# Kernel tuning notes

Measured on AMD Instinct MI355X. Metric: run time of the kernel, lower is better.

## Reference

```python
import jax, jax.numpy as jnp
import numpy as np

DIM = 384
HEADS = 12
CUBE = (4, 7, 7)
N = CUBE[0] * CUBE[1] * CUBE[2]  # 196
HIDDEN = 4 * DIM
BW = 256  # num_windows * batch
EPS = 1e-5


def _relative_position_index():
    c, h, w = CUBE
    coords = np.stack(np.meshgrid(np.arange(c), np.arange(h), np.arange(w), indexing='ij'))  # [3,c,h,w]
    flat = coords.reshape(3, -1)  # [3, N]
    rel = flat[:, :, None] - flat[:, None, :]  # [3, N, N]
    rel = rel.transpose(1, 2, 0).copy()
    rel[:, :, 0] += c - 1
    rel[:, :, 1] += h - 1
    rel[:, :, 2] += w - 1
    rel[:, :, 1] *= 2 * w - 1
    rel[:, :, 0] *= (2 * h - 1) * (2 * w - 1)
    return rel.sum(-1).astype(np.int32)  # [N, N]


def setup_inputs() -> dict:
    key = jax.random.key(0)
    ks = jax.random.split(key, 16)
    s = 0.02
    table_rows = (2 * CUBE[0] - 1) * (2 * CUBE[1] - 1) * (2 * CUBE[2] - 1)
    return {
        'x': jax.random.normal(ks[0], (BW, N, DIM), jnp.float32),
        'norm1_w': jnp.ones((DIM,), jnp.float32),
        'norm1_b': jnp.zeros((DIM,), jnp.float32),
        'qkv_w': jax.random.normal(ks[1], (DIM, 3 * DIM), jnp.float32) * s,
        'qkv_b': jnp.zeros((3 * DIM,), jnp.float32),
        'proj_w': jax.random.normal(ks[2], (DIM, DIM), jnp.float32) * s,
        'proj_b': jnp.zeros((DIM,), jnp.float32),
        'rpb_table': jax.random.normal(ks[3], (table_rows, HEADS), jnp.float32) * s,
        'norm2_w': jnp.ones((DIM,), jnp.float32),
        'norm2_b': jnp.zeros((DIM,), jnp.float32),
        'fc1_w': jax.random.normal(ks[4], (DIM, HIDDEN), jnp.float32) * s,
        'fc1_b': jnp.zeros((HIDDEN,), jnp.float32),
        'fc2_w': jax.random.normal(ks[5], (HIDDEN, DIM), jnp.float32) * s,
        'fc2_b': jnp.zeros((DIM,), jnp.float32),
        'rpi': jnp.asarray(_relative_position_index()),
    }


def _layernorm(x, w, b):
    mu = jnp.mean(x, axis=-1, keepdims=True)
    var = jnp.mean(jnp.square(x - mu), axis=-1, keepdims=True)
    return (x - mu) * jax.lax.rsqrt(var + EPS) * w + b


def reference(x, norm1_w, norm1_b, qkv_w, qkv_b, proj_w, proj_b, rpb_table,
              norm2_w, norm2_b, fc1_w, fc1_b, fc2_w, fc2_b, rpi):
    B_, n, C = x.shape
    hd = C // HEADS
    scale = hd ** (-0.5)

    # --- attention branch ---
    h = _layernorm(x, norm1_w, norm1_b)
    qkv = (h @ qkv_w + qkv_b).reshape(B_, n, 3, HEADS, hd)
    q, k, v = qkv[:, :, 0], qkv[:, :, 1], qkv[:, :, 2]  # [B_, n, H, hd]
    attn = jnp.einsum('bqhd,bkhd->bhqk', q * scale, k)
    bias = rpb_table[rpi]                 # [n, n, H]
    attn = attn + jnp.transpose(bias, (2, 0, 1))[None]
    attn = jax.nn.softmax(attn, axis=-1)
    out = jnp.einsum('bhqk,bkhd->bqhd', attn, v).reshape(B_, n, C)
    out = out @ proj_w + proj_b
    x = x + out

    # --- MLP branch ---
    h = _layernorm(x, norm2_w, norm2_b)
    h = jax.nn.gelu(h @ fc1_w + fc1_b, approximate=False)
    h = h @ fc2_w + fc2_b
    return x + h
```

## Files before the change

kernel.cpp:

```cpp
#include <hip/hip_runtime.h>
#include <hip/hip_bf16.h>
#include <math.h>

#define NDIM 384
#define NHEADS 12
#define NTOK 196
#define NBATCH 256
#define M_TOK (NBATCH * NTOK)
#define NHID 1536
#define THREE_DIM 1152
#define HD 32
#define EPSV 1e-5f
#define BH_STRIDE 7168
#define BPAD 224
#define LOG2E 1.4426950408889634f

typedef __hip_bfloat16 bf16;
typedef __attribute__((ext_vector_type(8))) short short8;
typedef __attribute__((ext_vector_type(4))) short short4v;
typedef __attribute__((ext_vector_type(4))) float f32x4;

__device__ __forceinline__ void gload_lds16(const void* g, void* l) {
  __builtin_amdgcn_global_load_lds((const __attribute__((address_space(1))) void*)g,
                                   (__attribute__((address_space(3))) void*)l, 16, 0, 0);
}

__global__ void k_transpose_bf16(const float* __restrict__ src, bf16* __restrict__ dst,
                                 int K, int N) {
  int idx = blockIdx.x * 256 + threadIdx.x;
  if (idx >= K * N) return;
  int k = idx / N, n = idx - k * N;
  dst[n * K + k] = __float2bfloat16(src[idx]);
}

__global__ void k_build_bias(const float* __restrict__ table, const int* __restrict__ rpi,
                             float* __restrict__ bias_pad) {
  int idx = blockIdx.x * 256 + threadIdx.x;
  if (idx >= NHEADS * BPAD * BPAD) return;
  int h = idx / (BPAD * BPAD);
  int rem = idx - h * (BPAD * BPAD);
  int r = rem / BPAD, c = rem - r * BPAD;
  float v;
  if (c >= NTOK) {
    v = -1e30f;
  } else {
    int rr = r < NTOK ? r : NTOK - 1;
    v = table[rpi[rr * NTOK + c] * NHEADS + h] * LOG2E;
  }
  bias_pad[idx] = v;
}

__global__ __launch_bounds__(256) void k_layernorm(const float* __restrict__ x,
                                                   const float* __restrict__ w,
                                                   const float* __restrict__ b,
                                                   bf16* __restrict__ out) {
  int token = blockIdx.x * 4 + (threadIdx.x >> 6);
  int lane = threadIdx.x & 63;
  const float* xr = x + (size_t)token * NDIM;
  float v[6];
  float s = 0.f;
#pragma unroll
  for (int i = 0; i < 6; ++i) { v[i] = xr[lane + i * 64]; s += v[i]; }
#pragma unroll
  for (int off = 32; off >= 1; off >>= 1) s += __shfl_xor(s, off);
  float mu = s * (1.f / NDIM);
  float s2 = 0.f;
#pragma unroll
  for (int i = 0; i < 6; ++i) { float d = v[i] - mu; s2 += d * d; }
#pragma unroll
  for (int off = 32; off >= 1; off >>= 1) s2 += __shfl_xor(s2, off);
  float r = rsqrtf(s2 * (1.f / NDIM) + EPSV);
  bf16* orow = out + (size_t)token * NDIM;
#pragma unroll
  for (int i = 0; i < 6; ++i) {
    int c = lane + i * 64;
    orow[c] = __float2bfloat16((v[i] - mu) * r * w[c] + b[c]);
  }
}

template <int EPI>
__device__ __forceinline__ void gemm_epilogue(const f32x4 acc[4][4], int m0, int n0,
                                              int lo, int hi,
                                              const float* __restrict__ bias,
                                              const float* __restrict__ resid,
                                              void* __restrict__ Cout,
                                              bf16* __restrict__ pq,
                                              bf16* __restrict__ pk,
                                              bf16* __restrict__ pv, int Nn) {
  const float qscale = 0.17677669529663687f * LOG2E;
#pragma unroll
  for (int i = 0; i < 4; ++i) {
    int r = m0 + i * 16 + lo;
#pragma unroll
    for (int j = 0; j < 4; ++j) {
      int cb0 = n0 + j * 16 + hi * 4;
      f32x4 bv = *(const f32x4*)(bias + cb0);
      f32x4 v;
#pragma unroll
      for (int e = 0; e < 4; ++e) v[e] = acc[i][j][e] + bv[e];
      if (EPI == 3) {
        int d0 = cb0 & 31;
        int hseg = cb0 >> 5;
        int which = hseg / 12;
        int h = hseg - which * 12;
        int b = r / 196;
        int t = r - b * 196;
        size_t base = (size_t)(b * 12 + h) * BH_STRIDE;
        if (which == 2) {
#pragma unroll
          for (int e = 0; e < 4; ++e)
            pv[base + (d0 + e) * BPAD + t] = __float2bfloat16(v[e]);
        } else if (which == 1) {
          union { short4v s; bf16 x[4]; } pack;
#pragma unroll
          for (int e = 0; e < 4; ++e) pack.x[e] = __float2bfloat16(v[e]);
          *(short4v*)(pk + base + t * 32 + d0) = pack.s;
        } else {
          union { short4v s; bf16 x[4]; } pack;
#pragma unroll
          for (int e = 0; e < 4; ++e) pack.x[e] = __float2bfloat16(v[e] * qscale);
          *(short4v*)(pq + base + t * 32 + d0) = pack.s;
        }
      } else if (EPI == 2) {
        size_t idx = (size_t)r * Nn + cb0;
        f32x4 rs = *(const f32x4*)(resid + idx);
#pragma unroll
        for (int e = 0; e < 4; ++e) v[e] += rs[e];
        *(f32x4*)((float*)Cout + idx) = v;
      } else {
        if (EPI == 1) {
#pragma unroll
          for (int e = 0; e < 4; ++e) {
            float val = v[e];
            float t = val * val;
            float p = __builtin_fmaf(0.044715f * val, t, val);
            float E = __expf(1.5957691216057308f * p);
            float rr = __builtin_amdgcn_rcpf(E + 1.f);
            v[e] = val - val * rr;
          }
        }
        union { short4v s; bf16 x[4]; } pack;
#pragma unroll
        for (int e = 0; e < 4; ++e) pack.x[e] = __float2bfloat16(v[e]);
        size_t idx = (size_t)r * Nn + cb0;
        *(short4v*)((bf16*)Cout + idx) = pack.s;
      }
    }
  }
}

template <int EPI>
__global__ __launch_bounds__(512) void k_gemm_bt(const bf16* __restrict__ A,
                                                 const bf16* __restrict__ Bt,
                                                 const float* __restrict__ bias,
                                                 const float* __restrict__ resid,
                                                 void* __restrict__ Cout,
                                                 bf16* __restrict__ pq,
                                                 bf16* __restrict__ pk,
                                                 bf16* __restrict__ pv,
                                                 int Nn, int K, int nbx) {
  __shared__ __align__(16) bf16 As[2][8192];
  __shared__ __align__(16) bf16 Bs[2][4096];
  const int tid = threadIdx.x;
  const int wave = tid >> 6, lane = tid & 63;
  const int lo = lane & 15, hi = lane >> 4;
  const int wm = wave >> 1, wn = wave & 1;

  const int nwg = gridDim.x;
  const int xcd = blockIdx.x & 7, bidx = blockIdx.x >> 3;
  const int q = nwg >> 3, rr8 = nwg & 7;
  const int swz = (xcd < rr8 ? xcd * (q + 1) : rr8 * (q + 1) + (xcd - rr8) * q) + bidx;
  const int m0 = (swz / nbx) * 256, n0 = (swz % nbx) * 128;

  f32x4 acc[4][4];
#pragma unroll
  for (int i = 0; i < 4; ++i)
#pragma unroll
    for (int j = 0; j < 4; ++j) acc[i][j] = (f32x4){0.f, 0.f, 0.f, 0.f};

  const int rowA0 = tid >> 2, part = tid & 3;
  const int sw = part ^ ((rowA0 >> 1) & 3);
  const bf16* ArowP0 = A + (size_t)(m0 + rowA0) * K + sw * 8;
  const bf16* ArowP1 = A + (size_t)(m0 + 128 + rowA0) * K + sw * 8;
  const bf16* BrowP = Bt + (size_t)(n0 + rowA0) * K + sw * 8;

#define STAGE(ks, abuf, bbuf)                                   \
  {                                                             \
    int k0_ = (ks) << 5;                                        \
    gload_lds16(ArowP0 + k0_, (abuf) + tid * 8);                \
    gload_lds16(ArowP1 + k0_, (abuf) + (512 + tid) * 8);        \
    gload_lds16(BrowP + k0_, (bbuf) + tid * 8);                 \
  }

  const int nk = K >> 5;
  STAGE(0, As[0], Bs[0]);
  __syncthreads();

  const int rsw = (lo >> 1) & 3;
  int cur = 0;
  for (int ks = 0; ks < nk; ++ks) {
    if (ks + 1 < nk) STAGE(ks + 1, As[cur ^ 1], Bs[cur ^ 1]);
    short8 af[4], bfr[4];
#pragma unroll
    for (int i = 0; i < 4; ++i) {
      af[i] = *(const short8*)(As[cur] + (wm * 64 + i * 16 + lo) * 32 + (hi ^ rsw) * 8);
      bfr[i] = *(const short8*)(Bs[cur] + (wn * 64 + i * 16 + lo) * 32 + (hi ^ rsw) * 8);
    }
#pragma unroll
    for (int i = 0; i < 4; ++i)
#pragma unroll
      for (int j = 0; j < 4; ++j)
        acc[i][j] = __builtin_amdgcn_mfma_f32_16x16x32_bf16(bfr[j], af[i], acc[i][j], 0, 0, 0);
    __syncthreads();
    cur ^= 1;
  }
#undef STAGE

  gemm_epilogue<EPI>(acc, m0 + wm * 64, n0 + wn * 64, lo, hi, bias, resid, Cout,
                     pq, pk, pv, Nn);
}

__global__ __launch_bounds__(256) void k_attn(const bf16* __restrict__ Qp,
                                              const bf16* __restrict__ Kp,
                                              const bf16* __restrict__ Vtp,
                                              const float* __restrict__ bias_pad,
                                              bf16* __restrict__ out) {
  __shared__ __align__(16) bf16 Ps[4][16][232];
  const int tid = threadIdx.x;
  const int wave = tid >> 6, lane = tid & 63;
  const int lo = lane & 15, hi = lane >> 4;
  const int nwg = gridDim.x;
  const int swz = (blockIdx.x & 7) * (nwg >> 3) + (blockIdx.x >> 3);
  const int unit = swz * 4 + wave;
  const int bh = unit / 13;
  const int qt = unit - bh * 13;
  const int h = bh % 12;
  const int b = bh / 12;
  const bf16* Qb = Qp + (size_t)bh * BH_STRIDE;
  const bf16* Kb = Kp + (size_t)bh * BH_STRIDE;
  const bf16* Vb = Vtp + (size_t)bh * BH_STRIDE;

  for (int i = lane; i < 256; i += 64)
    Ps[wave][i >> 4][208 + (i & 15)] = __float2bfloat16(0.f);

  short8 qf = *(const short8*)(Qb + (qt * 16 + lo) * 32 + hi * 8);

  f32x4 s[13];
  __builtin_amdgcn_s_setprio(1);
#pragma unroll
  for (int kt = 0; kt < 13; ++kt) {
    short8 kf = *(const short8*)(Kb + (kt * 16 + lo) * 32 + hi * 8);
    f32x4 z = {0.f, 0.f, 0.f, 0.f};
    s[kt] = __builtin_amdgcn_mfma_f32_16x16x32_bf16(qf, kf, z, 0, 0, 0);
  }
  __builtin_amdgcn_s_setprio(0);

  f32x4 inv;
#pragma unroll
  for (int e = 0; e < 4; ++e) {
    int qg = qt * 16 + hi * 4 + e;
    const float* brow = bias_pad + ((size_t)h * BPAD + qg) * BPAD;
    float sm = 0.f;
#pragma unroll
    for (int kt = 0; kt < 13; ++kt) {
      float pe = __builtin_amdgcn_exp2f(s[kt][e] + brow[kt * 16 + lo]);
      s[kt][e] = pe;
      sm += pe;
    }
#pragma unroll
    for (int off = 8; off >= 1; off >>= 1) sm += __shfl_xor(sm, off);
    inv[e] = 1.f / sm;
  }

#pragma unroll
  for (int kt = 0; kt < 13; ++kt) {
#pragma unroll
    for (int e = 0; e < 4; ++e)
      Ps[wave][hi * 4 + e][kt * 16 + lo] = __float2bfloat16(s[kt][e]);
  }

  f32x4 o[2] = {{0.f, 0.f, 0.f, 0.f}, {0.f, 0.f, 0.f, 0.f}};
  __builtin_amdgcn_s_setprio(1);
#pragma unroll
  for (int c = 0; c < 7; ++c) {
    short8 pa = *(const short8*)(&Ps[wave][lo][c * 32 + hi * 8]);
#pragma unroll
    for (int n = 0; n < 2; ++n) {
      short8 vf = *(const short8*)(Vb + (n * 16 + lo) * BPAD + c * 32 + hi * 8);
      o[n] = __builtin_amdgcn_mfma_f32_16x16x32_bf16(pa, vf, o[n], 0, 0, 0);
    }
  }
  __builtin_amdgcn_s_setprio(0);

#pragma unroll
  for (int n = 0; n < 2; ++n) {
#pragma unroll
    for (int e = 0; e < 4; ++e) {
      int qg = qt * 16 + hi * 4 + e;
      if (qg < NTOK)
        out[(size_t)(b * NTOK + qg) * NDIM + h * HD + n * 16 + lo] =
            __float2bfloat16(o[n][e] * inv[e]);
    }
  }
}

extern "C" void kernel_launch(void* const* d_in, const int* in_sizes, int n_in,
                              void* d_out, int out_size, void* d_ws, size_t ws_size,
                              hipStream_t stream) {
  const float* x       = (const float*)d_in[0];
  const float* norm1_w = (const float*)d_in[1];
  const float* norm1_b = (const float*)d_in[2];
  const float* qkv_w   = (const float*)d_in[3];
  const float* qkv_b   = (const float*)d_in[4];
  const float* proj_w  = (const float*)d_in[5];
  const float* proj_b  = (const float*)d_in[6];
  const float* rpb     = (const float*)d_in[7];
  const float* norm2_w = (const float*)d_in[8];
  const float* norm2_b = (const float*)d_in[9];
  const float* fc1_w   = (const float*)d_in[10];
  const float* fc1_b   = (const float*)d_in[11];
  const float* fc2_w   = (const float*)d_in[12];
  const float* fc2_b   = (const float*)d_in[13];
  const int*   rpi     = (const int*)d_in[14];
  float* out = (float*)d_out;

  char* ws = (char*)d_ws;
  bf16* pad_q = (bf16*)ws;
  bf16* pad_k = (bf16*)(ws + 44040192);
  bf16* pad_v = (bf16*)(ws + 2 * 44040192);
  float* bias_pad = (float*)(ws + 3 * 44040192);
  bf16* mlp1 = (bf16*)ws;
  bf16* hbuf = (bf16*)(ws + 154140672);
  bf16* wqkv_t = (bf16*)(ws + 154140672 + 38535168);
  bf16* wproj_t = wqkv_t + 442368;
  bf16* wfc1_t = wproj_t + 147456;
  bf16* wfc2_t = wfc1_t + 589824;

  k_transpose_bf16<<<(442368 + 255) / 256, 256, 0, stream>>>(qkv_w, wqkv_t, 384, 1152);
  k_transpose_bf16<<<(147456 + 255) / 256, 256, 0, stream>>>(proj_w, wproj_t, 384, 384);
  k_transpose_bf16<<<(589824 + 255) / 256, 256, 0, stream>>>(fc1_w, wfc1_t, 384, 1536);
  k_transpose_bf16<<<(589824 + 255) / 256, 256, 0, stream>>>(fc2_w, wfc2_t, 1536, 384);
  k_build_bias<<<(NHEADS * BPAD * BPAD + 255) / 256, 256, 0, stream>>>(rpb, rpi, bias_pad);

  k_layernorm<<<M_TOK / 4, 256, 0, stream>>>(x, norm1_w, norm1_b, hbuf);
  k_gemm_bt<3><<<196 * 9, 512, 0, stream>>>(hbuf, wqkv_t, qkv_b, nullptr, nullptr,
                                            pad_q, pad_k, pad_v, 1152, 384, 9);
  k_attn<<<9984, 256, 0, stream>>>(pad_q, pad_k, pad_v, bias_pad, hbuf);
  k_gemm_bt<2><<<196 * 3, 512, 0, stream>>>(hbuf, wproj_t, proj_b, x, out,
                                            nullptr, nullptr, nullptr, 384, 384, 3);
  k_layernorm<<<M_TOK / 4, 256, 0, stream>>>(out, norm2_w, norm2_b, hbuf);
  k_gemm_bt<1><<<196 * 12, 512, 0, stream>>>(hbuf, wfc1_t, fc1_b, nullptr, mlp1,
                                             nullptr, nullptr, nullptr, 1536, 384, 12);
  k_gemm_bt<2><<<196 * 3, 512, 0, stream>>>(mlp1, wfc2_t, fc2_b, out, out,
                                            nullptr, nullptr, nullptr, 384, 1536, 3);
}
```

Measured before the change: 506.1 us.

## Restructure GEMM main loop with 64-wide K tiles and interleaved staged prefetch

```diff
diff --git a/kernel.cpp b/kernel.cpp
--- a/kernel.cpp
+++ b/kernel.cpp
@@ -159,8 +159,8 @@
                                                  bf16* __restrict__ pk,
                                                  bf16* __restrict__ pv,
                                                  int Nn, int K, int nbx) {
-  __shared__ __align__(16) bf16 As[2][8192];
-  __shared__ __align__(16) bf16 Bs[2][4096];
+  __shared__ __align__(16) bf16 Al[2][256 * 64];
+  __shared__ __align__(16) bf16 Bl[2][128 * 64];
   const int tid = threadIdx.x;
   const int wave = tid >> 6, lane = tid & 63;
   const int lo = lane & 15, hi = lane >> 4;
@@ -178,43 +178,110 @@
 #pragma unroll
     for (int j = 0; j < 4; ++j) acc[i][j] = (f32x4){0.f, 0.f, 0.f, 0.f};
 
-  const int rowA0 = tid >> 2, part = tid & 3;
-  const int sw = part ^ ((rowA0 >> 1) & 3);
-  const bf16* ArowP0 = A + (size_t)(m0 + rowA0) * K + sw * 8;
-  const bf16* ArowP1 = A + (size_t)(m0 + 128 + rowA0) * K + sw * 8;
-  const bf16* BrowP = Bt + (size_t)(n0 + rowA0) * K + sw * 8;
-
-#define STAGE(ks, abuf, bbuf)                                   \
-  {                                                             \
-    int k0_ = (ks) << 5;                                        \
-    gload_lds16(ArowP0 + k0_, (abuf) + tid * 8);                \
-    gload_lds16(ArowP1 + k0_, (abuf) + (512 + tid) * 8);        \
-    gload_lds16(BrowP + k0_, (bbuf) + tid * 8);                 \
-  }
-
-  const int nk = K >> 5;
-  STAGE(0, As[0], Bs[0]);
-  __syncthreads();
-
-  const int rsw = (lo >> 1) & 3;
+  int offA[4], ldsA[4];
+#pragma unroll
+  for (int u = 0; u < 4; ++u) {
+    int ch = (u >> 1) * 1024 + ((wave * 2 + (u & 1)) * 64 + lane);
+    int row = ch >> 3, c = ch & 7;
+    offA[u] = (m0 + row) * K + ((c ^ (row & 7)) * 8);
+    ldsA[u] = ch * 8;
+  }
+  int offB[2], ldsB[2];
+#pragma unroll
+  for (int u = 0; u < 2; ++u) {
+    int ch = (wave * 2 + u) * 64 + lane;
+    int row = ch >> 3, c = ch & 7;
+    offB[u] = (n0 + row) * K + ((c ^ (row & 7)) * 8);
+    ldsB[u] = ch * 8;
+  }
+
+#define STG_B(k0_, buf)                                          \
+  { gload_lds16(Bt + (size_t)offB[0] + (k0_), Bl[buf] + ldsB[0]); \
+    gload_lds16(Bt + (size_t)offB[1] + (k0_), Bl[buf] + ldsB[1]); }
+#define STG_A0(k0_, buf)                                         \
+  { gload_lds16(A + (size_t)offA[0] + (k0_), Al[buf] + ldsA[0]); \
+    gload_lds16(A + (size_t)offA[1] + (k0_), Al[buf] + ldsA[1]); }
+#define STG_A1(k0_, buf)                                         \
+  { gload_lds16(A + (size_t)offA[2] + (k0_), Al[buf] + ldsA[2]); \
+    gload_lds16(A + (size_t)offA[3] + (k0_), Al[buf] + ldsA[3]); }
+
+  const int rsw = lo & 7;
+  const int aRow = (wm * 64 + lo) * 64;
+  const int bRow = (wn * 64 + lo) * 64;
+  const int cOff0 = ((hi) ^ rsw) * 8;
+  const int cOff1 = ((4 + hi) ^ rsw) * 8;
+
+  const int nt = K >> 6;
+  STG_B(0, 0);
+  STG_A0(0, 0);
+  STG_A1(0, 0);
+
   int cur = 0;
-  for (int ks = 0; ks < nk; ++ks) {
-    if (ks + 1 < nk) STAGE(ks + 1, As[cur ^ 1], Bs[cur ^ 1]);
-    short8 af[4], bfr[4];
-#pragma unroll
-    for (int i = 0; i < 4; ++i) {
-      af[i] = *(const short8*)(As[cur] + (wm * 64 + i * 16 + lo) * 32 + (hi ^ rsw) * 8);
-      bfr[i] = *(const short8*)(Bs[cur] + (wn * 64 + i * 16 + lo) * 32 + (hi ^ rsw) * 8);
-    }
-#pragma unroll
-    for (int i = 0; i < 4; ++i)
-#pragma unroll
-      for (int j = 0; j < 4; ++j)
-        acc[i][j] = __builtin_amdgcn_mfma_f32_16x16x32_bf16(bfr[j], af[i], acc[i][j], 0, 0, 0);
-    __syncthreads();
+  for (int t = 0; t < nt; ++t) {
+    const int kn = (t + 1) << 6;
+    const bool pf = (t + 1 < nt);
+    short8 bq[4], aq0, aq1;
+    if (pf) {
+      STG_B(kn, cur ^ 1);
+      asm volatile("s_waitcnt vmcnt(2)" ::: "memory");
+    } else {
+      asm volatile("s_waitcnt vmcnt(0)" ::: "memory");
+    }
+    __builtin_amdgcn_s_barrier();
+#pragma unroll
+    for (int j = 0; j < 4; ++j) bq[j] = *(const short8*)(Bl[cur] + bRow + j * 1024 + cOff0);
+    aq0 = *(const short8*)(Al[cur] + aRow + 0 + cOff0);
+    aq1 = *(const short8*)(Al[cur] + aRow + 1024 + cOff0);
+    __builtin_amdgcn_s_setprio(1);
+#pragma unroll
+    for (int j = 0; j < 4; ++j) {
+      acc[0][j] = __builtin_amdgcn_mfma_f32_16x16x32_bf16(bq[j], aq0, acc[0][j], 0, 0, 0);
+      acc[1][j] = __builtin_amdgcn_mfma_f32_16x16x32_bf16(bq[j], aq1, acc[1][j], 0, 0, 0);
+    }
+    __builtin_amdgcn_s_setprio(0);
+    __builtin_amdgcn_s_barrier();
+    aq0 = *(const short8*)(Al[cur] + aRow + 2048 + cOff0);
+    aq1 = *(const short8*)(Al[cur] + aRow + 3072 + cOff0);
+    if (pf) STG_A0(kn, cur ^ 1);
+    __builtin_amdgcn_s_barrier();
+    __builtin_amdgcn_s_setprio(1);
+#pragma unroll
+    for (int j = 0; j < 4; ++j) {
+      acc[2][j] = __builtin_amdgcn_mfma_f32_16x16x32_bf16(bq[j], aq0, acc[2][j], 0, 0, 0);
+      acc[3][j] = __builtin_amdgcn_mfma_f32_16x16x32_bf16(bq[j], aq1, acc[3][j], 0, 0, 0);
+    }
+    __builtin_amdgcn_s_setprio(0);
+    __builtin_amdgcn_s_barrier();
+#pragma unroll
+    for (int j = 0; j < 4; ++j) bq[j] = *(const short8*)(Bl[cur] + bRow + j * 1024 + cOff1);
+    aq0 = *(const short8*)(Al[cur] + aRow + 0 + cOff1);
+    aq1 = *(const short8*)(Al[cur] + aRow + 1024 + cOff1);
+    if (pf) STG_A1(kn, cur ^ 1);
+    __builtin_amdgcn_s_barrier();
+    __builtin_amdgcn_s_setprio(1);
+#pragma unroll
+    for (int j = 0; j < 4; ++j) {
+      acc[0][j] = __builtin_amdgcn_mfma_f32_16x16x32_bf16(bq[j], aq0, acc[0][j], 0, 0, 0);
+      acc[1][j] = __builtin_amdgcn_mfma_f32_16x16x32_bf16(bq[j], aq1, acc[1][j], 0, 0, 0);
+    }
+    __builtin_amdgcn_s_setprio(0);
+    __builtin_amdgcn_s_barrier();
+    aq0 = *(const short8*)(Al[cur] + aRow + 2048 + cOff1);
+    aq1 = *(const short8*)(Al[cur] + aRow + 3072 + cOff1);
+    __builtin_amdgcn_s_barrier();
+    __builtin_amdgcn_s_setprio(1);
+#pragma unroll
+    for (int j = 0; j < 4; ++j) {
+      acc[2][j] = __builtin_amdgcn_mfma_f32_16x16x32_bf16(bq[j], aq0, acc[2][j], 0, 0, 0);
+      acc[3][j] = __builtin_amdgcn_mfma_f32_16x16x32_bf16(bq[j], aq1, acc[3][j], 0, 0, 0);
+    }
+    __builtin_amdgcn_s_setprio(0);
+    __builtin_amdgcn_s_barrier();
     cur ^= 1;
   }
-#undef STAGE
+#undef STG_B
+#undef STG_A0
+#undef STG_A1
 
   gemm_epilogue<EPI>(acc, m0 + wm * 64, n0 + wn * 64, lo, hi, bias, resid, Cout,
                      pq, pk, pv, Nn);
```

After: 604.9 us. 1.2x slower.
